# Kernel tuning notes

Measured on AMD Instinct MI355X. Metric: run time of the kernel, lower is better.

## Reference

```python
import jax, jax.numpy as jnp
import numpy as np

EPS = 1e-6
ROPE_THETA = 1000000.0
SPAN_LENGTHS = [700, 300, 600, 448]
L, D, H, HK, DH, FF = 2, 2048, 16, 8, 128, 8192


def _rmsnorm(x, w):
    var = jnp.mean(jnp.square(x), axis=-1, keepdims=True)
    return x * jax.lax.rsqrt(var + EPS) * w


def _rotate_half(x):
    x1, x2 = jnp.split(x, 2, axis=-1)
    return jnp.concatenate([-x2, x1], axis=-1)


def setup_inputs() -> dict:
    key = jax.random.key(0)
    ks = jax.random.split(key, 8)
    s = 0.02  # init scale
    seg = np.repeat(np.arange(len(SPAN_LENGTHS), dtype=np.int32), SPAN_LENGTHS)
    pos = np.concatenate([np.arange(n, dtype=np.int32) for n in SPAN_LENGTHS])
    T = seg.shape[0]
    return {
        "hidden_states": jax.random.normal(ks[0], (T, D), jnp.float32),
        "ln1_w": jnp.ones((L, D), jnp.float32),
        "ln2_w": jnp.ones((L, D), jnp.float32),
        "wq": jax.random.normal(ks[1], (L, D, H * DH), jnp.float32) * s,
        "wk": jax.random.normal(ks[2], (L, D, HK * DH), jnp.float32) * s,
        "wv": jax.random.normal(ks[3], (L, D, HK * DH), jnp.float32) * s,
        "wo": jax.random.normal(ks[4], (L, H * DH, D), jnp.float32) * s,
        "qn_w": jnp.ones((L, DH), jnp.float32),
        "kn_w": jnp.ones((L, DH), jnp.float32),
        "wg": jax.random.normal(ks[5], (L, D, FF), jnp.float32) * s,
        "wu": jax.random.normal(ks[6], (L, D, FF), jnp.float32) * s,
        "wd": jax.random.normal(ks[7], (L, FF, D), jnp.float32) * s,
        "final_norm_w": jnp.ones((D,), jnp.float32),
        "segment_ids": jnp.asarray(seg),
        "position_ids": jnp.asarray(pos),
    }


def reference(hidden_states, ln1_w, ln2_w, wq, wk, wv, wo, qn_w, kn_w, wg, wu, wd, final_norm_w, segment_ids, position_ids):
    T = hidden_states.shape[0]
    # rotary tables from per-request positions (positions reset per span)
    inv_freq = 1.0 / (ROPE_THETA ** (jnp.arange(0, DH, 2, dtype=jnp.float32) / DH))
    freqs = position_ids.astype(jnp.float32)[:, None] * inv_freq  # [T, DH/2]
    emb = jnp.concatenate([freqs, freqs], axis=-1)                # [T, DH]
    cos = jnp.cos(emb)[:, None, :]
    sin = jnp.sin(emb)[:, None, :]
    # ragged causal mask: attend only within the same request span, causally
    tok = jnp.arange(T)
    mask = (segment_ids[:, None] == segment_ids[None, :]) & (tok[:, None] >= tok[None, :])
    neg = jnp.finfo(hidden_states.dtype).min
    scale = 1.0 / np.sqrt(DH)

    x = hidden_states
    for l in range(L):
        h = _rmsnorm(x, ln1_w[l])
        q = (h @ wq[l]).reshape(T, H, DH)
        k = (h @ wk[l]).reshape(T, HK, DH)
        v = (h @ wv[l]).reshape(T, HK, DH)
        q = _rmsnorm(q, qn_w[l])  # Qwen3 per-head q/k RMSNorm
        k = _rmsnorm(k, kn_w[l])
        q = q * cos + _rotate_half(q) * sin
        k = k * cos + _rotate_half(k) * sin
        rep = H // HK  # GQA
        k = jnp.repeat(k, rep, axis=1)
        v = jnp.repeat(v, rep, axis=1)
        scores = jnp.einsum('thd,shd->hts', q, k) * scale  # [H, T, T]
        scores = jnp.where(mask[None], scores, neg)
        attn = jax.nn.softmax(scores, axis=-1)
        o = jnp.einsum('hts,shd->thd', attn, v).reshape(T, H * DH)
        x = x + o @ wo[l]
        h = _rmsnorm(x, ln2_w[l])
        x = x + (jax.nn.silu(h @ wg[l]) * (h @ wu[l])) @ wd[l]
    return _rmsnorm(x, final_norm_w)
```

## Files before the change

### kernel.cpp

```cpp
#include <hip/hip_runtime.h>
#include <stdint.h>

#define T_SEQ 2048
#define DMODEL 2048
#define NH 16
#define NKV 8
#define DHEAD 128
#define DFF 8192

typedef float f32x4 __attribute__((ext_vector_type(4)));
typedef float f32x2 __attribute__((ext_vector_type(2)));
typedef __bf16 bf16x8 __attribute__((ext_vector_type(8)));
typedef unsigned short ushort_t;

typedef __attribute__((address_space(1))) void gvoid;
typedef __attribute__((address_space(3))) void lvoid;

__device__ inline unsigned short f2bf(float f) {
  unsigned int u = __float_as_uint(f);
  u += 0x7fffu + ((u >> 16) & 1u);
  return (unsigned short)(u >> 16);
}
__device__ inline float bf2f(unsigned short h) {
  return __uint_as_float(((unsigned int)h) << 16);
}

__device__ inline void gload_lds16(const void* g, void* l) {
  __builtin_amdgcn_global_load_lds((gvoid*)g, (lvoid*)l, 16, 0, 0);
}

template <typename TIN>
__global__ __launch_bounds__(256) void k_transpose_bf16(const TIN* __restrict__ in,
                                                        ushort_t* __restrict__ out,
                                                        int R, int C) {
  __shared__ float tile[64 * 72];
  int tid = threadIdx.x;
  int r0 = blockIdx.y * 64, c0 = blockIdx.x * 64;
  int rl = tid >> 4;
  int cc = tid & 15;
#pragma unroll
  for (int i = 0; i < 4; ++i) {
    int row = rl + i * 16;
    const TIN* src = in + (size_t)(r0 + row) * C + c0 + cc * 4;
    float v0, v1, v2, v3;
    if constexpr (sizeof(TIN) == 4) {
      f32x4 v = *(const f32x4*)src;
      v0 = v.x; v1 = v.y; v2 = v.z; v3 = v.w;
    } else {
      ushort4 v = *(const ushort4*)src;
      v0 = bf2f(v.x); v1 = bf2f(v.y); v2 = bf2f(v.z); v3 = bf2f(v.w);
    }
    int chunk = cc ^ (row & 15);
    f32x4 t = {v0, v1, v2, v3};
    *(f32x4*)&tile[row * 72 + chunk * 4] = t;
  }
  __syncthreads();
#pragma unroll
  for (int i = 0; i < 4; ++i) {
    int nrow = rl + i * 16;
    int k4 = cc * 4;
    ushort4 o;
    {
      int k = k4 + 0;
      o.x = f2bf(tile[k * 72 + (((nrow >> 2) ^ (k & 15)) << 2) + (nrow & 3)]);
      k = k4 + 1;
      o.y = f2bf(tile[k * 72 + (((nrow >> 2) ^ (k & 15)) << 2) + (nrow & 3)]);
      k = k4 + 2;
      o.z = f2bf(tile[k * 72 + (((nrow >> 2) ^ (k & 15)) << 2) + (nrow & 3)]);
      k = k4 + 3;
      o.w = f2bf(tile[k * 72 + (((nrow >> 2) ^ (k & 15)) << 2) + (nrow & 3)]);
    }
    *(ushort4*)(out + (size_t)(c0 + nrow) * R + r0 + k4) = o;
  }
}

template <int BF16OUT>
__global__ __launch_bounds__(256) void k_rmsnorm(const float* __restrict__ X,
                                                 const float* __restrict__ W,
                                                 void* __restrict__ OUT) {
  int row = blockIdx.x, tid = threadIdx.x;
  const float* xr = X + (size_t)row * DMODEL;
  f32x4 x0 = *(const f32x4*)(xr + tid * 4);
  f32x4 x1 = *(const f32x4*)(xr + 1024 + tid * 4);
  float ss = x0.x * x0.x + x0.y * x0.y + x0.z * x0.z + x0.w * x0.w +
             x1.x * x1.x + x1.y * x1.y + x1.z * x1.z + x1.w * x1.w;
#pragma unroll
  for (int o = 1; o < 64; o <<= 1) ss += __shfl_xor(ss, o, 64);
  __shared__ float red[4];
  int w = tid >> 6;
  if ((tid & 63) == 0) red[w] = ss;
  __syncthreads();
  float tot = red[0] + red[1] + red[2] + red[3];
  float sc = rsqrtf(tot / (float)DMODEL + 1e-6f);
  f32x4 w0 = *(const f32x4*)(W + tid * 4);
  f32x4 w1 = *(const f32x4*)(W + 1024 + tid * 4);
  if constexpr (BF16OUT) {
    ushort_t* o = (ushort_t*)OUT + (size_t)row * DMODEL;
    ushort4 a, b;
    a.x = f2bf(x0.x * sc * w0.x); a.y = f2bf(x0.y * sc * w0.y);
    a.z = f2bf(x0.z * sc * w0.z); a.w = f2bf(x0.w * sc * w0.w);
    b.x = f2bf(x1.x * sc * w1.x); b.y = f2bf(x1.y * sc * w1.y);
    b.z = f2bf(x1.z * sc * w1.z); b.w = f2bf(x1.w * sc * w1.w);
    *(ushort4*)(o + tid * 4) = a;
    *(ushort4*)(o + 1024 + tid * 4) = b;
  } else {
    float* o = (float*)OUT + (size_t)row * DMODEL;
    f32x4 a = {x0.x * sc * w0.x, x0.y * sc * w0.y, x0.z * sc * w0.z, x0.w * sc * w0.w};
    f32x4 b = {x1.x * sc * w1.x, x1.y * sc * w1.y, x1.z * sc * w1.z, x1.w * sc * w1.w};
    *(f32x4*)(o + tid * 4) = a;
    *(f32x4*)(o + 1024 + tid * 4) = b;
  }
}

__global__ __launch_bounds__(256) void k_red4res(const float* __restrict__ P,
                                                 const float* __restrict__ RES,
                                                 float* __restrict__ OUT, int n) {
  int i = (blockIdx.x * 256 + threadIdx.x) * 4;
  if (i >= n) return;
  f32x4 v = *(const f32x4*)(RES + i);
#pragma unroll
  for (int z = 0; z < 4; ++z) {
    f32x4 t = *(const f32x4*)(P + (size_t)z * n + i);
    v.x += t.x; v.y += t.y; v.z += t.z; v.w += t.w;
  }
  *(f32x4*)(OUT + i) = v;
}

#define EPI_STORE 0
#define EPI_SILU 2
#define EPI_STOREB 3

#define LOAD_B256(bs, rbase)                                                   \
  {                                                                            \
    _Pragma("unroll") for (int ks = 0; ks < 2; ++ks)                           \
        _Pragma("unroll") for (int ni = 0; ni < 2; ++ni)                       \
            bfr[ks][ni] = *(const bf16x8*)((bs) +                              \
                (((rbase) + ni * 16 + lr) << 6) +                              \
                ((((ks << 2) + lg) ^ (lr & 7)) << 3));                         \
  }

#define MFMA_Q256(q)                                                           \
  {                                                                            \
    _Pragma("unroll") for (int ks = 0; ks < 2; ++ks)                           \
        _Pragma("unroll") for (int mi = 0; mi < 4; ++mi)                       \
            _Pragma("unroll") for (int ni = 0; ni < 2; ++ni)                   \
                acc[mi][(q) * 2 + ni] =                                        \
                    __builtin_amdgcn_mfma_f32_16x16x32_bf16(                   \
                        af[ks][mi], bfr[ks][ni], acc[mi][(q) * 2 + ni], 0, 0, 0); \
  }

template <int LAST>
__device__ __forceinline__ void g256_iter(
    const ushort_t* __restrict__ as, const ushort_t* __restrict__ bsA,
    const ushort_t* __restrict__ bsB, ushort_t* __restrict__ nA,
    ushort_t* __restrict__ nB, const ushort_t* __restrict__ an,
    const ushort_t* __restrict__ bn, size_t rs, int slds, int lr, int lg,
    f32x4 (&acc)[4][8]) {
  bf16x8 af[2][4], bfr[2][2];
#pragma unroll
  for (int ks = 0; ks < 2; ++ks)
#pragma unroll
    for (int mi = 0; mi < 4; ++mi)
      af[ks][mi] = *(const bf16x8*)(as + ((mi * 16 + lr) << 6) +
                                    ((((ks << 2) + lg) ^ (lr & 7)) << 3));
  LOAD_B256(bsA, 0);
  if constexpr (!LAST) {
    gload_lds16(an, nA + slds);
    gload_lds16(an + rs, nA + 4096 + slds);
  }
  __builtin_amdgcn_s_barrier();
  asm volatile("s_waitcnt lgkmcnt(0)" ::: "memory");
  __builtin_amdgcn_sched_barrier(0);
  __builtin_amdgcn_s_setprio(1);
  MFMA_Q256(0);
  __builtin_amdgcn_s_setprio(0);
  __builtin_amdgcn_s_barrier();
  LOAD_B256(bsA, 32);
  if constexpr (!LAST) {
    gload_lds16(an + 2 * rs, nA + 8192 + slds);
    gload_lds16(an + 3 * rs, nA + 12288 + slds);
    asm volatile("s_waitcnt vmcnt(4)" ::: "memory");
  } else {
    asm volatile("s_waitcnt vmcnt(0)" ::: "memory");
  }
  __builtin_amdgcn_s_barrier();
  asm volatile("s_waitcnt lgkmcnt(0)" ::: "memory");
  __builtin_amdgcn_sched_barrier(0);
  __builtin_amdgcn_s_setprio(1);
  MFMA_Q256(1);
  __builtin_amdgcn_s_setprio(0);
  __builtin_amdgcn_s_barrier();
  LOAD_B256(bsB, 0);
  if constexpr (!LAST) {
    gload_lds16(bn, nB + slds);
    gload_lds16(bn + 2 * rs, nB + 8192 + slds);
  }
  __builtin_amdgcn_s_barrier();
  asm volatile("s_waitcnt lgkmcnt(0)" ::: "memory");
  __builtin_amdgcn_sched_barrier(0);
  __builtin_amdgcn_s_setprio(1);
  MFMA_Q256(2);
  __builtin_amdgcn_s_setprio(0);
  __builtin_amdgcn_s_barrier();
  LOAD_B256(bsB, 32);
  if constexpr (!LAST) {
    gload_lds16(bn + rs, nB + 4096 + slds);
    gload_lds16(bn + 3 * rs, nB + 12288 + slds);
    asm volatile("s_waitcnt vmcnt(2)" ::: "memory");
  }
  __builtin_amdgcn_s_barrier();
  asm volatile("s_waitcnt lgkmcnt(0)" ::: "memory");
  __builtin_amdgcn_sched_barrier(0);
  __builtin_amdgcn_s_setprio(1);
  MFMA_Q256(3);
  __builtin_amdgcn_s_setprio(0);
  __builtin_amdgcn_s_barrier();
}

template <int EPI>
__global__ __launch_bounds__(512, 2) void k_gemm256(
    const ushort_t* __restrict__ A, const ushort_t* __restrict__ BT,
    const ushort_t* __restrict__ GINB, float* __restrict__ CF,
    ushort_t* __restrict__ CB, int N, int Kstride, int Kc, size_t zoff) {
  __shared__ ushort_t lds[65536];
  const int tid = threadIdx.x;
  const int l = tid & 63, wid = tid >> 6;
  const int wm = wid >> 1, wn = wid & 1;
  const int lr = l & 15, lg = l >> 4;
  const int m0 = blockIdx.y * 256, n0 = blockIdx.x * 256;
  const int z = blockIdx.z;
  const int NT = Kc >> 6;

  A += (size_t)z * Kc;
  BT += (size_t)z * Kc;
  CF += (size_t)z * zoff;

  const int srow = tid >> 3;
  const int scs = (tid & 7) ^ (srow & 7);
  const size_t sgoff = (size_t)srow * Kstride + scs * 8;
  const int slds = wid * 512;

  const ushort_t* ga = A + (size_t)m0 * Kstride + sgoff;
  const ushort_t* gb = BT + (size_t)n0 * Kstride + sgoff;
  const size_t rs = (size_t)64 * Kstride;

  f32x4 acc[4][8] = {};

  ushort_t* Ab0 = lds;
  ushort_t* Bb0 = lds + 16384;
  ushort_t* Ab1 = lds + 32768;
  ushort_t* Bb1 = lds + 49152;

  gload_lds16(ga, Ab0 + slds);
  gload_lds16(ga + rs, Ab0 + 4096 + slds);
  gload_lds16(ga + 2 * rs, Ab0 + 8192 + slds);
  gload_lds16(ga + 3 * rs, Ab0 + 12288 + slds);
  gload_lds16(gb, Bb0 + slds);
  gload_lds16(gb + 2 * rs, Bb0 + 8192 + slds);
  gload_lds16(gb + rs, Bb0 + 4096 + slds);
  gload_lds16(gb + 3 * rs, Bb0 + 12288 + slds);
  asm volatile("s_waitcnt vmcnt(2)" ::: "memory");
  __builtin_amdgcn_s_barrier();

  for (int kt = 0; kt < NT - 1; ++kt) {
    const int d = kt & 1;
    const ushort_t* as = (d ? Ab1 : Ab0) + wm * 4096;
    const ushort_t* bsA = (d ? Bb1 : Bb0) + (wn * 2) * 4096;
    ushort_t* nA = d ? Ab0 : Ab1;
    ushort_t* nB = d ? Bb0 : Bb1;
    g256_iter<0>(as, bsA, bsA + 4096, nA, nB, ga + (size_t)(kt + 1) * 64,
                 gb + (size_t)(kt + 1) * 64, rs, slds, lr, lg, acc);
  }
  {
    const int d = (NT - 1) & 1;
    const ushort_t* as = (d ? Ab1 : Ab0) + wm * 4096;
    const ushort_t* bsA = (d ? Bb1 : Bb0) + (wn * 2) * 4096;
    g256_iter<1>(as, bsA, bsA + 4096, nullptr, nullptr, nullptr, nullptr, rs,
                 slds, lr, lg, acc);
  }

#pragma unroll
  for (int mi = 0; mi < 4; ++mi)
#pragma unroll
    for (int ci = 0; ci < 8; ++ci)
#pragma unroll
      for (int rr = 0; rr < 4; ++rr) {
        int m = m0 + wm * 64 + mi * 16 + lg * 4 + rr;
        int n = n0 + wn * 128 + ci * 16 + lr;
        size_t off = (size_t)m * N + n;
        float v = acc[mi][ci][rr];
        if constexpr (EPI == EPI_STORE) {
          CF[off] = v;
        } else if constexpr (EPI == EPI_STOREB) {
          CB[off] = f2bf(v);
        } else {
          float gv = bf2f(GINB[off]);
          float s = gv / (1.f + __expf(-gv));
          CB[off] = f2bf(s * v);
        }
      }
}

__global__ __launch_bounds__(256) void k_qkv_post(const float* __restrict__ Q0,
                                                  const float* __restrict__ Q1,
                                                  const float* __restrict__ QNW,
                                                  const float* __restrict__ KNW,
                                                  const int* __restrict__ POS,
                                                  ushort_t* __restrict__ Qb,
                                                  ushort_t* __restrict__ Kb,
                                                  ushort_t* __restrict__ Vb) {
  int t = blockIdx.x;
  int tid = threadIdx.x;
  int w = tid >> 6, l = tid & 63;
  float pos = (float)POS[t];
  const float* base0 = Q0 + (size_t)t * 4096;
  const float* base1 = Q1 + (size_t)t * 4096;
  int i0 = 2 * (l & 31);
  const float K2 = 19.931568569324174f / 64.f;
  float ang0 = pos * exp2f(-(float)i0 * K2);
  float ang1 = pos * exp2f(-(float)(i0 + 1) * K2);
  float cs0 = cosf(ang0), sn0 = sinf(ang0);
  float cs1 = cosf(ang1), sn1 = sinf(ang1);
#pragma unroll
  for (int si = 0; si < 8; ++si) {
    int slot = w + si * 4;
    f32x2 xa = *(const f32x2*)(base0 + slot * 128 + l * 2);
    f32x2 xb = *(const f32x2*)(base1 + slot * 128 + l * 2);
    float v0 = xa.x + xb.x, v1 = xa.y + xb.y;
    float ss = v0 * v0 + v1 * v1;
#pragma unroll
    for (int o = 1; o < 64; o <<= 1) ss += __shfl_xor(ss, o, 64);
    if (slot < 24) {
      float sc = rsqrtf(ss / 128.f + 1e-6f);
      const float* wn = (slot < 16) ? QNW : KNW;
      f32x2 wv = *(const f32x2*)(wn + l * 2);
      v0 = v0 * sc * wv.x;
      v1 = v1 * sc * wv.y;
      float p0 = __shfl_xor(v0, 32, 64);
      float p1 = __shfl_xor(v1, 32, 64);
      float r0 = (l < 32) ? -p0 : p0;
      float r1 = (l < 32) ? -p1 : p1;
      v0 = v0 * cs0 + r0 * sn0;
      v1 = v1 * cs1 + r1 * sn1;
    }
    ushort2 uv;
    uv.x = f2bf(v0);
    uv.y = f2bf(v1);
    ushort_t* dst;
    if (slot < 16)
      dst = Qb + (size_t)t * 2048 + slot * 128 + l * 2;
    else if (slot < 24)
      dst = Kb + (size_t)t * 1024 + (slot - 16) * 128 + l * 2;
    else
      dst = Vb + (size_t)t * 1024 + (slot - 24) * 128 + l * 2;
    *(ushort2*)dst = uv;
  }
}

__global__ __launch_bounds__(64) void k_flash(const ushort_t* __restrict__ Qb,
                                              const ushort_t* __restrict__ Kb,
                                              const ushort_t* __restrict__ VT,
                                              const int* __restrict__ SEG,
                                              ushort_t* __restrict__ Ob) {
  __shared__ ushort_t Pl[16 * 40];
  int l = threadIdx.x;
  int qt = blockIdx.x, h = blockIdx.y;
  int q0 = qt * 16;
  int lr = l & 15, lg = l >> 4;
  int kvh = h >> 1;
  bf16x8 qf[4];
  {
    const bf16x8* qv = (const bf16x8*)(Qb + (size_t)(q0 + lr) * 2048 + h * 128);
#pragma unroll
    for (int kk = 0; kk < 4; ++kk) qf[kk] = qv[kk * 4 + lg];
  }
  int segq[4];
#pragma unroll
  for (int r = 0; r < 4; ++r) segq[r] = SEG[q0 + lg * 4 + r];
  int target = SEG[q0];
  int lo = 0, hi = q0;
  while (lo < hi) {
    int mid = (lo + hi) >> 1;
    if (SEG[mid] < target) lo = mid + 1; else hi = mid;
  }
  int s_start = lo & ~31;
  float m_run[4], l_run[4];
  f32x4 acc[8] = {};
#pragma unroll
  for (int r = 0; r < 4; ++r) { m_run[r] = -1e30f; l_run[r] = 0.f; }
  const float scale = 0.08838834764831845f;
  for (int s0 = s_start; s0 < q0 + 16; s0 += 32) {
    int sa = s0 + lr, sb = s0 + 16 + lr;
    int sac = min(sa, T_SEQ - 1), sbc = min(sb, T_SEQ - 1);
    f32x4 SA = {}, SB = {};
    const bf16x8* ka = (const bf16x8*)(Kb + (size_t)sac * 1024 + kvh * 128);
    const bf16x8* kb = (const bf16x8*)(Kb + (size_t)sbc * 1024 + kvh * 128);
#pragma unroll
    for (int kk = 0; kk < 4; ++kk) {
      SA = __builtin_amdgcn_mfma_f32_16x16x32_bf16(qf[kk], ka[kk * 4 + lg], SA, 0, 0, 0);
      SB = __builtin_amdgcn_mfma_f32_16x16x32_bf16(qf[kk], kb[kk * 4 + lg], SB, 0, 0, 0);
    }
    int sga = SEG[sac], sgb = SEG[sbc];
    float al[4], pA[4], pB[4];
#pragma unroll
    for (int r = 0; r < 4; ++r) {
      int qrow = q0 + lg * 4 + r;
      float xa = (sa <= qrow && sga == segq[r]) ? SA[r] * scale : -1e30f;
      float xb = (sb <= qrow && sgb == segq[r]) ? SB[r] * scale : -1e30f;
      float mx = fmaxf(xa, xb);
#pragma unroll
      for (int o = 1; o < 16; o <<= 1) mx = fmaxf(mx, __shfl_xor(mx, o, 64));
      float nm = fmaxf(m_run[r], mx);
      float ea = __expf(xa - nm), eb = __expf(xb - nm);
      float rs = ea + eb;
#pragma unroll
      for (int o = 1; o < 16; o <<= 1) rs += __shfl_xor(rs, o, 64);
      al[r] = __expf(m_run[r] - nm);
      l_run[r] = l_run[r] * al[r] + rs;
      m_run[r] = nm;
      pA[r] = ea;
      pB[r] = eb;
    }
#pragma unroll
    for (int c = 0; c < 8; ++c)
#pragma unroll
      for (int r = 0; r < 4; ++r) acc[c][r] *= al[r];
    __syncthreads();
#pragma unroll
    for (int r = 0; r < 4; ++r) {
      Pl[(lg * 4 + r) * 40 + lr] = f2bf(pA[r]);
      Pl[(lg * 4 + r) * 40 + 16 + lr] = f2bf(pB[r]);
    }
    __syncthreads();
    bf16x8 pa = *(const bf16x8*)&Pl[lr * 40 + lg * 8];
    int sbase = min(s0 + lg * 8, T_SEQ - 8);
#pragma unroll
    for (int c = 0; c < 8; ++c) {
      bf16x8 vb = *(const bf16x8*)(VT + (size_t)(kvh * 128 + c * 16 + lr) * T_SEQ + sbase);
      acc[c] = __builtin_amdgcn_mfma_f32_16x16x32_bf16(pa, vb, acc[c], 0, 0, 0);
    }
  }
#pragma unroll
  for (int c = 0; c < 8; ++c)
#pragma unroll
    for (int r = 0; r < 4; ++r) {
      float ov = acc[c][r] / l_run[r];
      Ob[(size_t)(q0 + lg * 4 + r) * 2048 + h * 128 + c * 16 + lr] = f2bf(ov);
    }
}

extern "C" void kernel_launch(void* const* d_in, const int* in_sizes, int n_in,
                              void* d_out, int out_size, void* d_ws, size_t ws_size,
                              hipStream_t stream) {
  const float* hidden = (const float*)d_in[0];
  const float* ln1 = (const float*)d_in[1];
  const float* ln2 = (const float*)d_in[2];
  const float* wq = (const float*)d_in[3];
  const float* wk = (const float*)d_in[4];
  const float* wv = (const float*)d_in[5];
  const float* wo = (const float*)d_in[6];
  const float* qnw = (const float*)d_in[7];
  const float* knw = (const float*)d_in[8];
  const float* wg = (const float*)d_in[9];
  const float* wu = (const float*)d_in[10];
  const float* wd = (const float*)d_in[11];
  const float* fnw = (const float*)d_in[12];
  const int* seg = (const int*)d_in[13];
  const int* pos = (const int*)d_in[14];
  float* out = (float*)d_out;

  char* ws = (char*)d_ws;
  size_t off = 0;
  auto alloc = [&](size_t bytes) {
    char* p = ws + off;
    off += (bytes + 255) & ~(size_t)255;
    return p;
  };
  ushort_t* wT = (ushort_t*)alloc((size_t)DFF * DMODEL * 2);
  ushort_t* hbuf = (ushort_t*)alloc((size_t)T_SEQ * DMODEL * 2);
  ushort_t* qb = (ushort_t*)alloc((size_t)T_SEQ * 2048 * 2);
  ushort_t* kb = (ushort_t*)alloc((size_t)T_SEQ * 1024 * 2);
  ushort_t* vb = (ushort_t*)alloc((size_t)T_SEQ * 1024 * 2);
  ushort_t* vT = (ushort_t*)alloc((size_t)T_SEQ * 1024 * 2);
  ushort_t* ob = (ushort_t*)alloc((size_t)T_SEQ * 2048 * 2);
  float* gbufF = (float*)alloc((size_t)T_SEQ * DFF * 4);
  ushort_t* gbufB = (ushort_t*)gbufF;
  ushort_t* mbuf = (ushort_t*)alloc((size_t)T_SEQ * DFF * 2);
  (void)ws_size; (void)in_sizes; (void)n_in; (void)out_size;

  dim3 b256(256), b64(64), b512(512);
  for (int lyr = 0; lyr < 2; ++lyr) {
    const float* xsrc = (lyr == 0) ? hidden : out;
    k_rmsnorm<1><<<T_SEQ, b256, 0, stream>>>(xsrc, ln1 + (size_t)lyr * DMODEL, hbuf);

    const float* wql = wq + (size_t)lyr * DMODEL * 2048;
    const float* wkl = wk + (size_t)lyr * DMODEL * 1024;
    const float* wvl = wv + (size_t)lyr * DMODEL * 1024;
    k_transpose_bf16<float><<<dim3(32, 32), b256, 0, stream>>>(wql, wT, 2048, 2048);
    k_transpose_bf16<float><<<dim3(16, 32), b256, 0, stream>>>(wkl, wT + (size_t)2048 * 2048, 2048, 1024);
    k_transpose_bf16<float><<<dim3(16, 32), b256, 0, stream>>>(wvl, wT + (size_t)3072 * 2048, 2048, 1024);
    k_gemm256<EPI_STORE><<<dim3(16, 8, 2), b512, 0, stream>>>(
        hbuf, wT, nullptr, gbufF, nullptr, 4096, 2048, 1024, (size_t)2048 * 4096);
    k_qkv_post<<<T_SEQ, b256, 0, stream>>>(gbufF, gbufF + (size_t)2048 * 4096,
                                           qnw + (size_t)lyr * 128, knw + (size_t)lyr * 128,
                                           pos, qb, kb, vb);
    k_transpose_bf16<ushort_t><<<dim3(16, 32), b256, 0, stream>>>(vb, vT, 2048, 1024);
    k_flash<<<dim3(T_SEQ / 16, NH), b64, 0, stream>>>(qb, kb, vT, seg, ob);

    const float* wol = wo + (size_t)lyr * 2048 * DMODEL;
    k_transpose_bf16<float><<<dim3(32, 32), b256, 0, stream>>>(wol, wT, 2048, 2048);
    k_gemm256<EPI_STORE><<<dim3(8, 8, 4), b512, 0, stream>>>(
        ob, wT, nullptr, gbufF, nullptr, 2048, 2048, 512, (size_t)2048 * 2048);
    k_red4res<<<4096, b256, 0, stream>>>(gbufF, xsrc, out, 2048 * 2048);

    k_rmsnorm<1><<<T_SEQ, b256, 0, stream>>>(out, ln2 + (size_t)lyr * DMODEL, hbuf);

    const float* wgl = wg + (size_t)lyr * DMODEL * DFF;
    const float* wul = wu + (size_t)lyr * DMODEL * DFF;
    const float* wdl = wd + (size_t)lyr * DFF * DMODEL;
    k_transpose_bf16<float><<<dim3(128, 32), b256, 0, stream>>>(wgl, wT, 2048, 8192);
    k_gemm256<EPI_STOREB><<<dim3(32, 8, 1), b512, 0, stream>>>(
        hbuf, wT, nullptr, nullptr, gbufB, 8192, 2048, 2048, 0);
    k_transpose_bf16<float><<<dim3(128, 32), b256, 0, stream>>>(wul, wT, 2048, 8192);
    k_gemm256<EPI_SILU><<<dim3(32, 8, 1), b512, 0, stream>>>(
        hbuf, wT, gbufB, nullptr, mbuf, 8192, 2048, 2048, 0);
    k_transpose_bf16<float><<<dim3(32, 128), b256, 0, stream>>>(wdl, wT, 8192, 2048);
    k_gemm256<EPI_STORE><<<dim3(8, 8, 4), b512, 0, stream>>>(
        mbuf, wT, nullptr, gbufF, nullptr, 2048, 8192, 2048, (size_t)2048 * 2048);
    k_red4res<<<4096, b256, 0, stream>>>(gbufF, out, out, 2048 * 2048);
  }
  k_rmsnorm<0><<<T_SEQ, b256, 0, stream>>>(out, fnw, out);
}
```

Measured before the change: 986.0 us.

## Fuse QK-norm and RoPE into QKV GEMM epilogue; share K/V across GQA heads

The QKV GEMM no longer splits K across two z-slices into fp32 partials. It runs full-K and applies per-head RMSNorm and rotary embedding directly in its epilogue, writing bf16 Q/K/V. This removes the separate post-processing kernel and the fp32 round trip through memory. The flash attention kernel now processes both query heads of a GQA pair per block, reusing K and V loads. It also prefetches V before the score MFMAs and drops the block barriers around the P staging. In exchange, the QKV grid has half as many blocks, the epilogue does more per-thread transcendental work, and the attention kernel uses more registers.

```diff
diff --git a/kernel.cpp b/kernel.cpp
--- a/kernel.cpp
+++ b/kernel.cpp
@@ -129,6 +129,7 @@
 #define EPI_STORE 0
 #define EPI_SILU 2
 #define EPI_STOREB 3
+#define EPI_QKV 4
 
 #define LOAD_B256(bs, rbase)                                                   \
   {                                                                            \
@@ -221,7 +222,10 @@
 __global__ __launch_bounds__(512, 2) void k_gemm256(
     const ushort_t* __restrict__ A, const ushort_t* __restrict__ BT,
     const ushort_t* __restrict__ GINB, float* __restrict__ CF,
-    ushort_t* __restrict__ CB, int N, int Kstride, int Kc, size_t zoff) {
+    ushort_t* __restrict__ CB, int N, int Kstride, int Kc, size_t zoff,
+    const float* __restrict__ QNW, const float* __restrict__ KNW,
+    const int* __restrict__ POS, ushort_t* __restrict__ Qb,
+    ushort_t* __restrict__ Kb, ushort_t* __restrict__ Vb) {
   __shared__ ushort_t lds[65536];
   const int tid = threadIdx.x;
   const int l = tid & 63, wid = tid >> 6;
@@ -279,81 +283,82 @@
                  slds, lr, lg, acc);
   }
 
-#pragma unroll
-  for (int mi = 0; mi < 4; ++mi)
-#pragma unroll
-    for (int ci = 0; ci < 8; ++ci)
-#pragma unroll
-      for (int rr = 0; rr < 4; ++rr) {
-        int m = m0 + wm * 64 + mi * 16 + lg * 4 + rr;
-        int n = n0 + wn * 128 + ci * 16 + lr;
-        size_t off = (size_t)m * N + n;
-        float v = acc[mi][ci][rr];
-        if constexpr (EPI == EPI_STORE) {
-          CF[off] = v;
-        } else if constexpr (EPI == EPI_STOREB) {
-          CB[off] = f2bf(v);
-        } else {
-          float gv = bf2f(GINB[off]);
-          float s = gv / (1.f + __expf(-gv));
-          CB[off] = f2bf(s * v);
+  if constexpr (EPI == EPI_QKV) {
+    const int head = (n0 >> 7) + wn;
+    if (head < 24) {
+      const float* nw = (head < 16) ? QNW : KNW;
+      float w_lo[4], w_hi[4], ifr[4];
+      const float k2c = 19.931568569324174f / 64.f;
+#pragma unroll
+      for (int ci = 0; ci < 4; ++ci) {
+        int dd = ci * 16 + lr;
+        w_lo[ci] = nw[dd];
+        w_hi[ci] = nw[dd + 64];
+        ifr[ci] = exp2f(-(float)dd * k2c);
+      }
+#pragma unroll
+      for (int mi = 0; mi < 4; ++mi)
+#pragma unroll
+        for (int rr = 0; rr < 4; ++rr) {
+          int m = m0 + wm * 64 + mi * 16 + lg * 4 + rr;
+          float vals[8];
+          float ssum = 0.f;
+#pragma unroll
+          for (int ci = 0; ci < 8; ++ci) {
+            vals[ci] = acc[mi][ci][rr];
+            ssum += vals[ci] * vals[ci];
+          }
+#pragma unroll
+          for (int o = 1; o < 16; o <<= 1) ssum += __shfl_xor(ssum, o, 64);
+          float scn = rsqrtf(ssum * (1.f / 128.f) + 1e-6f);
+          float pf = (float)POS[m];
+          ushort_t o16[8];
+#pragma unroll
+          for (int ci = 0; ci < 4; ++ci) {
+            float a = vals[ci] * scn * w_lo[ci];
+            float b = vals[ci + 4] * scn * w_hi[ci];
+            float th = pf * ifr[ci];
+            float cs = cosf(th), sn = sinf(th);
+            o16[ci] = f2bf(a * cs - b * sn);
+            o16[ci + 4] = f2bf(b * cs + a * sn);
+          }
+          ushort_t* dst = (head < 16) ? (Qb + (size_t)m * 2048 + head * 128)
+                                      : (Kb + (size_t)m * 1024 + (head - 16) * 128);
+#pragma unroll
+          for (int ci = 0; ci < 8; ++ci) dst[ci * 16 + lr] = o16[ci];
         }
-      }
-}
-
-__global__ __launch_bounds__(256) void k_qkv_post(const float* __restrict__ Q0,
-                                                  const float* __restrict__ Q1,
-                                                  const float* __restrict__ QNW,
-                                                  const float* __restrict__ KNW,
-                                                  const int* __restrict__ POS,
-                                                  ushort_t* __restrict__ Qb,
-                                                  ushort_t* __restrict__ Kb,
-                                                  ushort_t* __restrict__ Vb) {
-  int t = blockIdx.x;
-  int tid = threadIdx.x;
-  int w = tid >> 6, l = tid & 63;
-  float pos = (float)POS[t];
-  const float* base0 = Q0 + (size_t)t * 4096;
-  const float* base1 = Q1 + (size_t)t * 4096;
-  int i0 = 2 * (l & 31);
-  const float K2 = 19.931568569324174f / 64.f;
-  float ang0 = pos * exp2f(-(float)i0 * K2);
-  float ang1 = pos * exp2f(-(float)(i0 + 1) * K2);
-  float cs0 = cosf(ang0), sn0 = sinf(ang0);
-  float cs1 = cosf(ang1), sn1 = sinf(ang1);
-#pragma unroll
-  for (int si = 0; si < 8; ++si) {
-    int slot = w + si * 4;
-    f32x2 xa = *(const f32x2*)(base0 + slot * 128 + l * 2);
-    f32x2 xb = *(const f32x2*)(base1 + slot * 128 + l * 2);
-    float v0 = xa.x + xb.x, v1 = xa.y + xb.y;
-    float ss = v0 * v0 + v1 * v1;
-#pragma unroll
-    for (int o = 1; o < 64; o <<= 1) ss += __shfl_xor(ss, o, 64);
-    if (slot < 24) {
-      float sc = rsqrtf(ss / 128.f + 1e-6f);
-      const float* wn = (slot < 16) ? QNW : KNW;
-      f32x2 wv = *(const f32x2*)(wn + l * 2);
-      v0 = v0 * sc * wv.x;
-      v1 = v1 * sc * wv.y;
-      float p0 = __shfl_xor(v0, 32, 64);
-      float p1 = __shfl_xor(v1, 32, 64);
-      float r0 = (l < 32) ? -p0 : p0;
-      float r1 = (l < 32) ? -p1 : p1;
-      v0 = v0 * cs0 + r0 * sn0;
-      v1 = v1 * cs1 + r1 * sn1;
-    }
-    ushort2 uv;
-    uv.x = f2bf(v0);
-    uv.y = f2bf(v1);
-    ushort_t* dst;
-    if (slot < 16)
-      dst = Qb + (size_t)t * 2048 + slot * 128 + l * 2;
-    else if (slot < 24)
-      dst = Kb + (size_t)t * 1024 + (slot - 16) * 128 + l * 2;
-    else
-      dst = Vb + (size_t)t * 1024 + (slot - 24) * 128 + l * 2;
-    *(ushort2*)dst = uv;
+    } else {
+#pragma unroll
+      for (int mi = 0; mi < 4; ++mi)
+#pragma unroll
+        for (int rr = 0; rr < 4; ++rr) {
+          int m = m0 + wm * 64 + mi * 16 + lg * 4 + rr;
+          ushort_t* dst = Vb + (size_t)m * 1024 + (head - 24) * 128;
+#pragma unroll
+          for (int ci = 0; ci < 8; ++ci) dst[ci * 16 + lr] = f2bf(acc[mi][ci][rr]);
+        }
+    }
+  } else {
+#pragma unroll
+    for (int mi = 0; mi < 4; ++mi)
+#pragma unroll
+      for (int ci = 0; ci < 8; ++ci)
+#pragma unroll
+        for (int rr = 0; rr < 4; ++rr) {
+          int m = m0 + wm * 64 + mi * 16 + lg * 4 + rr;
+          int n = n0 + wn * 128 + ci * 16 + lr;
+          size_t off = (size_t)m * N + n;
+          float v = acc[mi][ci][rr];
+          if constexpr (EPI == EPI_STORE) {
+            CF[off] = v;
+          } else if constexpr (EPI == EPI_STOREB) {
+            CB[off] = f2bf(v);
+          } else if constexpr (EPI == EPI_SILU) {
+            float gv = bf2f(GINB[off]);
+            float s = gv / (1.f + __expf(-gv));
+            CB[off] = f2bf(s * v);
+          }
+        }
   }
 }
 
@@ -362,17 +367,20 @@
                                               const ushort_t* __restrict__ VT,
                                               const int* __restrict__ SEG,
                                               ushort_t* __restrict__ Ob) {
-  __shared__ ushort_t Pl[16 * 40];
+  __shared__ ushort_t Pl[2][16 * 40];
   int l = threadIdx.x;
-  int qt = blockIdx.x, h = blockIdx.y;
+  int qt = blockIdx.x, kvh = blockIdx.y;
   int q0 = qt * 16;
   int lr = l & 15, lg = l >> 4;
-  int kvh = h >> 1;
-  bf16x8 qf[4];
+  int h0 = kvh * 2;
+  bf16x8 qf0[4], qf1[4];
   {
-    const bf16x8* qv = (const bf16x8*)(Qb + (size_t)(q0 + lr) * 2048 + h * 128);
-#pragma unroll
-    for (int kk = 0; kk < 4; ++kk) qf[kk] = qv[kk * 4 + lg];
+    const bf16x8* qv = (const bf16x8*)(Qb + (size_t)(q0 + lr) * 2048 + h0 * 128);
+#pragma unroll
+    for (int kk = 0; kk < 4; ++kk) {
+      qf0[kk] = qv[kk * 4 + lg];
+      qf1[kk] = qv[16 + kk * 4 + lg];
+    }
   }
   int segq[4];
 #pragma unroll
@@ -384,69 +392,84 @@
     if (SEG[mid] < target) lo = mid + 1; else hi = mid;
   }
   int s_start = lo & ~31;
-  float m_run[4], l_run[4];
-  f32x4 acc[8] = {};
-#pragma unroll
-  for (int r = 0; r < 4; ++r) { m_run[r] = -1e30f; l_run[r] = 0.f; }
+  float mr[2][4], lrun[2][4];
+  f32x4 acc[2][8] = {};
+#pragma unroll
+  for (int h = 0; h < 2; ++h)
+#pragma unroll
+    for (int r = 0; r < 4; ++r) { mr[h][r] = -1e30f; lrun[h][r] = 0.f; }
   const float scale = 0.08838834764831845f;
   for (int s0 = s_start; s0 < q0 + 16; s0 += 32) {
     int sa = s0 + lr, sb = s0 + 16 + lr;
     int sac = min(sa, T_SEQ - 1), sbc = min(sb, T_SEQ - 1);
-    f32x4 SA = {}, SB = {};
+    bf16x8 vfr[8];
+    int sbase = min(s0 + lg * 8, T_SEQ - 8);
+#pragma unroll
+    for (int c = 0; c < 8; ++c)
+      vfr[c] = *(const bf16x8*)(VT + (size_t)(kvh * 128 + c * 16 + lr) * T_SEQ + sbase);
+    f32x4 SA0 = {}, SB0 = {}, SA1 = {}, SB1 = {};
     const bf16x8* ka = (const bf16x8*)(Kb + (size_t)sac * 1024 + kvh * 128);
-    const bf16x8* kb = (const bf16x8*)(Kb + (size_t)sbc * 1024 + kvh * 128);
+    const bf16x8* kb_ = (const bf16x8*)(Kb + (size_t)sbc * 1024 + kvh * 128);
 #pragma unroll
     for (int kk = 0; kk < 4; ++kk) {
-      SA = __builtin_amdgcn_mfma_f32_16x16x32_bf16(qf[kk], ka[kk * 4 + lg], SA, 0, 0, 0);
-      SB = __builtin_amdgcn_mfma_f32_16x16x32_bf16(qf[kk], kb[kk * 4 + lg], SB, 0, 0, 0);
+      bf16x8 kaf = ka[kk * 4 + lg];
+      bf16x8 kbf = kb_[kk * 4 + lg];
+      SA0 = __builtin_amdgcn_mfma_f32_16x16x32_bf16(qf0[kk], kaf, SA0, 0, 0, 0);
+      SB0 = __builtin_amdgcn_mfma_f32_16x16x32_bf16(qf0[kk], kbf, SB0, 0, 0, 0);
+      SA1 = __builtin_amdgcn_mfma_f32_16x16x32_bf16(qf1[kk], kaf, SA1, 0, 0, 0);
+      SB1 = __builtin_amdgcn_mfma_f32_16x16x32_bf16(qf1[kk], kbf, SB1, 0, 0, 0);
     }
     int sga = SEG[sac], sgb = SEG[sbc];
-    float al[4], pA[4], pB[4];
+    bool mAv[4], mBv[4];
 #pragma unroll
     for (int r = 0; r < 4; ++r) {
       int qrow = q0 + lg * 4 + r;
-      float xa = (sa <= qrow && sga == segq[r]) ? SA[r] * scale : -1e30f;
-      float xb = (sb <= qrow && sgb == segq[r]) ? SB[r] * scale : -1e30f;
-      float mx = fmaxf(xa, xb);
-#pragma unroll
-      for (int o = 1; o < 16; o <<= 1) mx = fmaxf(mx, __shfl_xor(mx, o, 64));
-      float nm = fmaxf(m_run[r], mx);
-      float ea = __expf(xa - nm), eb = __expf(xb - nm);
-      float rs = ea + eb;
-#pragma unroll
-      for (int o = 1; o < 16; o <<= 1) rs += __shfl_xor(rs, o, 64);
-      al[r] = __expf(m_run[r] - nm);
-      l_run[r] = l_run[r] * al[r] + rs;
-      m_run[r] = nm;
-      pA[r] = ea;
-      pB[r] = eb;
-    }
+      mAv[r] = (sa <= qrow) && (sga == segq[r]);
+      mBv[r] = (sb <= qrow) && (sgb == segq[r]);
+    }
+#pragma unroll
+    for (int h = 0; h < 2; ++h) {
+#pragma unroll
+      for (int r = 0; r < 4; ++r) {
+        float sva = (h ? SA1[r] : SA0[r]);
+        float svb = (h ? SB1[r] : SB0[r]);
+        float xa = mAv[r] ? sva * scale : -1e30f;
+        float xb = mBv[r] ? svb * scale : -1e30f;
+        float mx = fmaxf(xa, xb);
+#pragma unroll
+        for (int o = 1; o < 16; o <<= 1) mx = fmaxf(mx, __shfl_xor(mx, o, 64));
+        float nm = fmaxf(mr[h][r], mx);
+        float ea = __expf(xa - nm), eb = __expf(xb - nm);
+        float rsum = ea + eb;
+#pragma unroll
+        for (int o = 1; o < 16; o <<= 1) rsum += __shfl_xor(rsum, o, 64);
+        float al = __expf(mr[h][r] - nm);
+        lrun[h][r] = lrun[h][r] * al + rsum;
+        mr[h][r] = nm;
+#pragma unroll
+        for (int c = 0; c < 8; ++c) acc[h][c][r] *= al;
+        Pl[h][(lg * 4 + r) * 40 + lr] = f2bf(ea);
+        Pl[h][(lg * 4 + r) * 40 + 16 + lr] = f2bf(eb);
+      }
+    }
+    asm volatile("s_waitcnt lgkmcnt(0)" ::: "memory");
+    bf16x8 pa0 = *(const bf16x8*)&Pl[0][lr * 40 + lg * 8];
+    bf16x8 pa1 = *(const bf16x8*)&Pl[1][lr * 40 + lg * 8];
+#pragma unroll
+    for (int c = 0; c < 8; ++c) {
+      acc[0][c] = __builtin_amdgcn_mfma_f32_16x16x32_bf16(pa0, vfr[c], acc[0][c], 0, 0, 0);
+      acc[1][c] = __builtin_amdgcn_mfma_f32_16x16x32_bf16(pa1, vfr[c], acc[1][c], 0, 0, 0);
+    }
+  }
+#pragma unroll
+  for (int h = 0; h < 2; ++h)
 #pragma unroll
     for (int c = 0; c < 8; ++c)
 #pragma unroll
-      for (int r = 0; r < 4; ++r) acc[c][r] *= al[r];
-    __syncthreads();
-#pragma unroll
-    for (int r = 0; r < 4; ++r) {
-      Pl[(lg * 4 + r) * 40 + lr] = f2bf(pA[r]);
-      Pl[(lg * 4 + r) * 40 + 16 + lr] = f2bf(pB[r]);
-    }
-    __syncthreads();
-    bf16x8 pa = *(const bf16x8*)&Pl[lr * 40 + lg * 8];
-    int sbase = min(s0 + lg * 8, T_SEQ - 8);
-#pragma unroll
-    for (int c = 0; c < 8; ++c) {
-      bf16x8 vb = *(const bf16x8*)(VT + (size_t)(kvh * 128 + c * 16 + lr) * T_SEQ + sbase);
-      acc[c] = __builtin_amdgcn_mfma_f32_16x16x32_bf16(pa, vb, acc[c], 0, 0, 0);
-    }
-  }
-#pragma unroll
-  for (int c = 0; c < 8; ++c)
-#pragma unroll
-    for (int r = 0; r < 4; ++r) {
-      float ov = acc[c][r] / l_run[r];
-      Ob[(size_t)(q0 + lg * 4 + r) * 2048 + h * 128 + c * 16 + lr] = f2bf(ov);
-    }
+      for (int r = 0; r < 4; ++r) {
+        float ov = acc[h][c][r] / lrun[h][r];
+        Ob[(size_t)(q0 + lg * 4 + r) * 2048 + (h0 + h) * 128 + c * 16 + lr] = f2bf(ov);
+      }
 }
 
 extern "C" void kernel_launch(void* const* d_in, const int* in_sizes, int n_in,
@@ -499,18 +522,17 @@
     k_transpose_bf16<float><<<dim3(32, 32), b256, 0, stream>>>(wql, wT, 2048, 2048);
     k_transpose_bf16<float><<<dim3(16, 32), b256, 0, stream>>>(wkl, wT + (size_t)2048 * 2048, 2048, 1024);
     k_transpose_bf16<float><<<dim3(16, 32), b256, 0, stream>>>(wvl, wT + (size_t)3072 * 2048, 2048, 1024);
-    k_gemm256<EPI_STORE><<<dim3(16, 8, 2), b512, 0, stream>>>(
-        hbuf, wT, nullptr, gbufF, nullptr, 4096, 2048, 1024, (size_t)2048 * 4096);
-    k_qkv_post<<<T_SEQ, b256, 0, stream>>>(gbufF, gbufF + (size_t)2048 * 4096,
-                                           qnw + (size_t)lyr * 128, knw + (size_t)lyr * 128,
-                                           pos, qb, kb, vb);
+    k_gemm256<EPI_QKV><<<dim3(16, 8, 1), b512, 0, stream>>>(
+        hbuf, wT, nullptr, nullptr, nullptr, 4096, 2048, 2048, 0,
+        qnw + (size_t)lyr * 128, knw + (size_t)lyr * 128, pos, qb, kb, vb);
     k_transpose_bf16<ushort_t><<<dim3(16, 32), b256, 0, stream>>>(vb, vT, 2048, 1024);
-    k_flash<<<dim3(T_SEQ / 16, NH), b64, 0, stream>>>(qb, kb, vT, seg, ob);
+    k_flash<<<dim3(T_SEQ / 16, NKV), b64, 0, stream>>>(qb, kb, vT, seg, ob);
 
     const float* wol = wo + (size_t)lyr * 2048 * DMODEL;
     k_transpose_bf16<float><<<dim3(32, 32), b256, 0, stream>>>(wol, wT, 2048, 2048);
     k_gemm256<EPI_STORE><<<dim3(8, 8, 4), b512, 0, stream>>>(
-        ob, wT, nullptr, gbufF, nullptr, 2048, 2048, 512, (size_t)2048 * 2048);
+        ob, wT, nullptr, gbufF, nullptr, 2048, 2048, 512, (size_t)2048 * 2048,
+        nullptr, nullptr, nullptr, nullptr, nullptr, nullptr);
     k_red4res<<<4096, b256, 0, stream>>>(gbufF, xsrc, out, 2048 * 2048);
 
     k_rmsnorm<1><<<T_SEQ, b256, 0, stream>>>(out, ln2 + (size_t)lyr * DMODEL, hbuf);
@@ -520,13 +542,16 @@
     const float* wdl = wd + (size_t)lyr * DFF * DMODEL;
     k_transpose_bf16<float><<<dim3(128, 32), b256, 0, stream>>>(wgl, wT, 2048, 8192);
     k_gemm256<EPI_STOREB><<<dim3(32, 8, 1), b512, 0, stream>>>(
-        hbuf, wT, nullptr, nullptr, gbufB, 8192, 2048, 2048, 0);
+        hbuf, wT, nullptr, nullptr, gbufB, 8192, 2048, 2048, 0,
+        nullptr, nullptr, nullptr, nullptr, nullptr, nullptr);
     k_transpose_bf16<float><<<dim3(128, 32), b256, 0, stream>>>(wul, wT, 2048, 8192);
     k_gemm256<EPI_SILU><<<dim3(32, 8, 1), b512, 0, stream>>>(
-        hbuf, wT, gbufB, nullptr, mbuf, 8192, 2048, 2048, 0);
+        hbuf, wT, gbufB, nullptr, mbuf, 8192, 2048, 2048, 0,
+        nullptr, nullptr, nullptr, nullptr, nullptr, nullptr);
     k_transpose_bf16<float><<<dim3(32, 128), b256, 0, stream>>>(wdl, wT, 8192, 2048);
     k_gemm256<EPI_STORE><<<dim3(8, 8, 4), b512, 0, stream>>>(
-        mbuf, wT, nullptr, gbufF, nullptr, 2048, 8192, 2048, (size_t)2048 * 2048);
+        mbuf, wT, nullptr, gbufF, nullptr, 2048, 8192, 2048, (size_t)2048 * 2048,
+        nullptr, nullptr, nullptr, nullptr, nullptr, nullptr);
     k_red4res<<<4096, b256, 0, stream>>>(gbufF, out, out, 2048 * 2048);
   }
   k_rmsnorm<0><<<T_SEQ, b256, 0, stream>>>(out, fnw, out);
```

After: 1.062 ms. +7.7%, slower.
